# Optimization experiments

Hardware: AMD Instinct MI355X
Metric: run time of the kernel (lower is better)

## Reference

```python
import jax, jax.numpy as jnp
import numpy as np


def _conv_bn_relu(x, w, b, stride):
    # Conv2d(k=3, pad=1) with eval-mode BatchNorm folded into (w, b) at setup, then ReLU.
    y = jax.lax.conv_general_dilated(x, w, (stride, stride), ((1, 1), (1, 1)),
                                     dimension_numbers=('NCHW', 'OIHW', 'NCHW'))
    return jax.nn.relu(y + b[None, :, None, None])


def _affine_grid(theta, H, W):
    # torch.nn.functional.affine_grid, align_corners=False
    xs = (2.0 * jnp.arange(W, dtype=theta.dtype) + 1.0) / W - 1.0  # [W]
    ys = (2.0 * jnp.arange(H, dtype=theta.dtype) + 1.0) / H - 1.0  # [H]
    gx = theta[:, 0, 0, None, None] * xs[None, None, :] + theta[:, 0, 1, None, None] * ys[None, :, None] + theta[:, 0, 2, None, None]
    gy = theta[:, 1, 0, None, None] * xs[None, None, :] + theta[:, 1, 1, None, None] * ys[None, :, None] + theta[:, 1, 2, None, None]
    return jnp.stack([gx, gy], axis=-1)  # [B,H,W,2]


def _grid_sample_bilinear_zeros(im, grid):
    # torch.nn.functional.grid_sample, mode='bilinear', padding_mode='zeros', align_corners=False
    B, C, H, W = im.shape
    ix = ((grid[..., 0] + 1.0) * W - 1.0) * 0.5  # [B,H,W] pixel x coords
    iy = ((grid[..., 1] + 1.0) * H - 1.0) * 0.5
    x0 = jnp.floor(ix); y0 = jnp.floor(iy)
    x1 = x0 + 1.0;      y1 = y0 + 1.0
    wx1 = ix - x0; wx0 = 1.0 - wx1
    wy1 = iy - y0; wy0 = 1.0 - wy1
    imt = jnp.transpose(im, (0, 2, 3, 1))  # BHWC for channel-last gather
    bidx = jnp.arange(B)[:, None, None]

    def gather(xf, yf):
        valid = ((xf >= 0) & (xf <= W - 1) & (yf >= 0) & (yf <= H - 1)).astype(im.dtype)
        xi = jnp.clip(xf.astype(jnp.int32), 0, W - 1)
        yi = jnp.clip(yf.astype(jnp.int32), 0, H - 1)
        return imt[bidx, yi, xi] * valid[..., None]  # [B,H,W,C]

    out = (gather(x0, y0) * (wx0 * wy0)[..., None]
           + gather(x1, y0) * (wx1 * wy0)[..., None]
           + gather(x0, y1) * (wx0 * wy1)[..., None]
           + gather(x1, y1) * (wx1 * wy1)[..., None])
    return jnp.transpose(out, (0, 3, 1, 2))  # back to NCHW


def _forward(im_tensor, w1, b1, w2, b2, w3, b3, w4, b4, w5, b5, w6, b6,
             fw1, fb1, fw2, fb2, fw3, fb3):
    B, _, H, W = im_tensor.shape
    x1 = _conv_bn_relu(im_tensor, w1, b1, 1)
    x2 = _conv_bn_relu(jnp.concatenate([x1, im_tensor], 1), w2, b2, 2)
    x3 = _conv_bn_relu(x2, w3, b3, 1)
    x4 = _conv_bn_relu(jnp.concatenate([x3, x2], 1), w4, b4, 2)
    x5 = _conv_bn_relu(x4, w5, b5, 1)
    xs = _conv_bn_relu(jnp.concatenate([x5, x4], 1), w6, b6, 2)
    xs = xs.reshape(B, -1)  # [B, 24*(H/8)*(W/8)]
    h = jax.nn.relu(xs @ fw1.T + fb1)
    h = jax.nn.relu(h @ fw2.T + fb2)
    sz = h @ fw3.T + fb3  # [B, 4]
    # mode == 'normal': vectorized theta construction (original loops over batch)
    theta = jnp.zeros((B, 2, 3), dtype=im_tensor.dtype)
    theta = theta.at[:, 0, 0].set(jax.nn.sigmoid(sz[:, 0]))
    theta = theta.at[:, 0, 2].set(jnp.tanh(sz[:, 2]))
    theta = theta.at[:, 1, 1].set(jax.nn.sigmoid(sz[:, 1]))
    theta = theta.at[:, 1, 2].set(jnp.tanh(sz[:, 3]))
    grid = _affine_grid(theta, H, W)
    im_cropped = _grid_sample_bilinear_zeros(im_tensor, grid)
    return im_cropped, theta


def setup_inputs() -> dict:
    key = jax.random.key(0)
    B, H, W = 32, 256, 256
    keys = iter(jax.random.split(key, 64))
    nk = lambda: next(keys)
    im = jax.random.normal(nk(), (B, 1, H, W), jnp.float32)

    def conv_params(cin, cout):
        w = jax.random.normal(nk(), (cout, cin, 3, 3), jnp.float32) * (1.0 / np.sqrt(cin * 9))
        b = jax.random.normal(nk(), (cout,), jnp.float32) * 0.01
        # eval-mode BatchNorm params, folded into conv weight/bias (exact same math)
        gamma = 1.0 + 0.1 * jax.random.normal(nk(), (cout,), jnp.float32)
        beta = 0.1 * jax.random.normal(nk(), (cout,), jnp.float32)
        mean = 0.1 * jax.random.normal(nk(), (cout,), jnp.float32)
        var = jnp.abs(1.0 + 0.1 * jax.random.normal(nk(), (cout,), jnp.float32))
        scale = gamma / jnp.sqrt(var + 1e-5)
        return w * scale[:, None, None, None], b * scale + (beta - mean * scale)

    w1, b1 = conv_params(1, 8)
    w2, b2 = conv_params(9, 8)
    w3, b3 = conv_params(8, 16)
    w4, b4 = conv_params(24, 16)
    w5, b5 = conv_params(16, 24)
    w6, b6 = conv_params(40, 24)
    feat = 24 * (H // 8) * (W // 8)
    fw1 = jax.random.normal(nk(), (1024, feat), jnp.float32) * (1.0 / np.sqrt(feat))
    fb1 = jnp.zeros((1024,), jnp.float32)
    fw2 = jax.random.normal(nk(), (32, 1024), jnp.float32) * (1.0 / np.sqrt(1024))
    fb2 = jnp.zeros((32,), jnp.float32)
    fw3 = jax.random.normal(nk(), (4, 32), jnp.float32) * 0.01  # small perturbation of zero-init
    fb3 = jnp.array([1.0, 1.0, 0.0, 0.0], jnp.float32)
    return dict(im_tensor=im, w1=w1, b1=b1, w2=w2, b2=b2, w3=w3, b3=b3,
                w4=w4, b4=b4, w5=w5, b5=b5, w6=w6, b6=b6,
                fw1=fw1, fb1=fb1, fw2=fw2, fb2=fb2, fw3=fw3, fb3=fb3)


def reference(im_tensor, w1, b1, w2, b2, w3, b3, w4, b4, w5, b5, w6, b6,
              fw1, fb1, fw2, fb2, fw3, fb3):
    return _forward(im_tensor, w1, b1, w2, b2, w3, b3, w4, b4, w5, b5, w6, b6,
                    fw1, fb1, fw2, fb2, fw3, fb3)
```

## Files before the change

kernel.cpp:

```cpp
#include <hip/hip_runtime.h>
#include <hip/hip_bf16.h>

template <int CIN1, int CIN2, int COUT, int CG, int STRIDE, int CCH, int MINW>
__global__ __launch_bounds__(256, MINW) void conv2p_k(
    const float* __restrict__ in1, const float* __restrict__ in2,
    const float* __restrict__ w,
    const float* __restrict__ bias,
    float* __restrict__ out,
    int Hin, int Win)
{
    constexpr int CIN = CIN1 + CIN2;
    constexpr int NG  = COUT / CG;
    constexpr int NCH = CIN / CCH;
    constexpr int P   = 16 * STRIDE + 2;
    constexpr int NF4 = (STRIDE == 1) ? 10 : 17;
    constexpr int WL  = NF4 * 4;
    constexpr int E4  = CCH * P * NF4;
    constexpr int NLD = (E4 + 255) / 256;
    __shared__ __align__(16) float Xs[2][CCH][P][WL];

    const int Ho = Hin / STRIDE, Wo = Win / STRIDE;
    const int tpr = Wo / 32, tpc = Ho / 16;
    int bid = blockIdx.x;
    const int tx = bid % tpr; bid /= tpr;
    const int ty = bid % tpc; bid /= tpc;
    const int g  = bid % NG;  bid /= NG;
    const int b  = bid;
    const int cbase = g * CG;

    const int tid = threadIdx.x;
    const int lx = tid & 15, ly = tid >> 4;

    const int y0 = ty * 16 * STRIDE - 1;
    const int xA = tx * 32 * STRIDE - 4;
    const int HW = Hin * Win;

    float2 acc[CG];
#pragma unroll
    for (int co = 0; co < CG; ++co) {
        float bv = bias[cbase + co];
        acc[co].x = bv; acc[co].y = bv;
    }

    int cA[NLD], lOff[NLD], em[NLD];
    bool eok[NLD], rowk[NLD], f4[NLD];
    const float* b1p[NLD];
    const float* b2p[NLD];
#pragma unroll
    for (int l = 0; l < NLD; ++l) {
        int e = tid + l * 256;
        eok[l] = (e < E4);
        int ee = eok[l] ? e : 0;
        int c  = ee / (P * NF4), r = ee % (P * NF4);
        int py = r / NF4,        jx = r % NF4;
        cA[l]   = c;
        lOff[l] = ee;
        int gy = y0 + py, c0 = xA + jx * 4;
        rowk[l] = eok[l] && ((unsigned)gy < (unsigned)Hin);
        f4[l]   = (c0 >= 0) && (c0 + 4 <= Win);
        em[l] = 0;
#pragma unroll
        for (int e2 = 0; e2 < 4; ++e2)
            if ((unsigned)(c0 + e2) < (unsigned)Win) em[l] |= 1 << e2;
        b1p[l] = (const float*)((const char*)in1 +
                 ((ptrdiff_t)(b * CIN1 + c) * HW + (ptrdiff_t)gy * Win + c0)
                 * (ptrdiff_t)sizeof(float));
        b2p[l] = (CIN2 > 0)
            ? (const float*)((const char*)in2 +
                 ((ptrdiff_t)(b * CIN2 + c - CIN1) * HW + (ptrdiff_t)gy * Win + c0)
                 * (ptrdiff_t)sizeof(float))
            : b1p[l];
    }

    float4 stg[NLD];

    auto issue = [&](int cc) {
        const size_t adv = (size_t)cc * HW;
#pragma unroll
        for (int l = 0; l < NLD; ++l) {
            float4 v = {0.0f, 0.0f, 0.0f, 0.0f};
            if (rowk[l]) {
                int ci = cc + cA[l];
                const float* p = (CIN2 == 0 || ci < CIN1) ? (b1p[l] + adv)
                                                          : (b2p[l] + adv);
                if (f4[l]) {
                    v = *(const float4*)p;
                } else {
                    float* vp = reinterpret_cast<float*>(&v);
#pragma unroll
                    for (int e2 = 0; e2 < 4; ++e2)
                        if (em[l] & (1 << e2)) vp[e2] = p[e2];
                }
            }
            stg[l] = v;
        }
    };
    auto commit = [&](int bf) {
        float4* dst = (float4*)&Xs[0][0][0][0] + (size_t)bf * (CCH * P * NF4);
#pragma unroll
        for (int l = 0; l < NLD; ++l)
            if (eok[l]) dst[lOff[l]] = stg[l];
    };

    issue(0);
    commit(0);
    __syncthreads();

    const int cb = (2 * lx) * STRIDE + 3;

    int buf = 0;
    for (int ch = 0; ch < NCH; ++ch) {
        if (ch + 1 < NCH) issue((ch + 1) * CCH);
#pragma unroll
        for (int c = 0; c < CCH; ++c) {
#pragma unroll
            for (int ky = 0; ky < 3; ++ky) {
                const float* xr = &Xs[buf][c][ly * STRIDE + ky][0];
                float2 r0, r1, r2;
                r0.x = xr[cb + 0]; r0.y = xr[cb + 0 + STRIDE];
                r1.x = xr[cb + 1]; r1.y = xr[cb + 1 + STRIDE];
                r2.x = xr[cb + 2]; r2.y = xr[cb + 2 + STRIDE];
#pragma unroll
                for (int co = 0; co < CG; ++co) {
                    const float* wp = w +
                        ((size_t)(cbase + co) * CIN + ch * CCH + c) * 9 + ky * 3;
                    float w0 = wp[0], w1 = wp[1], w2 = wp[2];
                    float2 a = acc[co];
                    a.x = fmaf(r0.x, w0, a.x); a.y = fmaf(r0.y, w0, a.y);
                    a.x = fmaf(r1.x, w1, a.x); a.y = fmaf(r1.y, w1, a.y);
                    a.x = fmaf(r2.x, w2, a.x); a.y = fmaf(r2.y, w2, a.y);
                    acc[co] = a;
                }
            }
        }
        if (ch + 1 < NCH) {
            commit(buf ^ 1);
            __syncthreads();
            buf ^= 1;
        }
    }

    const int oy = ty * 16 + ly;
    const int ox = tx * 32 + 2 * lx;
#pragma unroll
    for (int co = 0; co < CG; ++co) {
        float2 v;
        v.x = fmaxf(acc[co].x, 0.0f);
        v.y = fmaxf(acc[co].y, 0.0f);
        *(float2*)&out[((size_t)(b * COUT + cbase + co) * Ho + oy) * Wo + ox] = v;
    }
}

#define FC1_K 24576
#define FC1_N 1024
#define FC1_M 32
#define FC1_KS 32
#define FC1_KC 768
#define FC1_KP 64
#define FC1_NT 64

__global__ __launch_bounds__(256) void fc1_stage_k(
    const float* __restrict__ xs,
    const float* __restrict__ fw1,
    float* __restrict__ part)
{
    __shared__ __align__(16) float As[FC1_KP][36];
    __shared__ __align__(16) float Bs[FC1_KP][66];

    const int tid = threadIdx.x;
    const int n0 = blockIdx.x * FC1_NT;
    const int ks = blockIdx.y;
    const int k0 = ks * FC1_KC;
    const int lane = tid & 63;
    const int grp = tid >> 6;

    const int m4 = (tid & 7) * 4;
    const int n2 = (tid >> 3) * 2;

    float acc[4][2];
#pragma unroll
    for (int i = 0; i < 4; ++i)
#pragma unroll
        for (int j = 0; j < 2; ++j) acc[i][j] = 0.0f;

    for (int p = 0; p < FC1_KC / FC1_KP; ++p) {
        const int kc = k0 + p * FC1_KP;
#pragma unroll
        for (int r = 0; r < 8; ++r) {
            int m = grp * 8 + r;
            As[lane][m] = xs[(size_t)m * FC1_K + kc + lane];
        }
#pragma unroll
        for (int r = 0; r < 16; ++r) {
            int nl = grp * 16 + r;
            Bs[lane][nl] = fw1[(size_t)(n0 + nl) * FC1_K + kc + lane];
        }
        __syncthreads();
#pragma unroll 8
        for (int k = 0; k < FC1_KP; ++k) {
            float4 a = *(const float4*)&As[k][m4];
            float2 bv = *(const float2*)&Bs[k][n2];
            acc[0][0] += a.x * bv.x; acc[0][1] += a.x * bv.y;
            acc[1][0] += a.y * bv.x; acc[1][1] += a.y * bv.y;
            acc[2][0] += a.z * bv.x; acc[2][1] += a.z * bv.y;
            acc[3][0] += a.w * bv.x; acc[3][1] += a.w * bv.y;
        }
        __syncthreads();
    }
#pragma unroll
    for (int i = 0; i < 4; ++i)
#pragma unroll
        for (int j = 0; j < 2; ++j)
            part[((size_t)ks * FC1_M + (m4 + i)) * FC1_N + n0 + n2 + j] = acc[i][j];
}

__global__ __launch_bounds__(256) void fc1_reduce_k(
    const float* __restrict__ part, const float* __restrict__ fb1,
    float* __restrict__ h1)
{
    int idx = blockIdx.x * 256 + threadIdx.x;
    int n = idx & (FC1_N - 1);
    int m = idx >> 10;
    float s = fb1[n];
#pragma unroll
    for (int ks = 0; ks < FC1_KS; ++ks)
        s += part[((size_t)ks * FC1_M + m) * FC1_N + n];
    h1[idx] = fmaxf(s, 0.0f);
}

__global__ __launch_bounds__(256) void fc2_k(
    const float* __restrict__ h1, const float* __restrict__ fw2,
    const float* __restrict__ fb2, float* __restrict__ h2)
{
    __shared__ float hs[1024];
    const int m = blockIdx.x;
    const int tid = threadIdx.x;
    for (int i = tid; i < 1024; i += 256) hs[i] = h1[m * 1024 + i];
    __syncthreads();
    const int wave = tid >> 6, lane = tid & 63;
#pragma unroll 1
    for (int nn = 0; nn < 8; ++nn) {
        int n = wave * 8 + nn;
        float p = 0.0f;
        for (int k = lane; k < 1024; k += 64)
            p += fw2[n * 1024 + k] * hs[k];
#pragma unroll
        for (int off = 32; off; off >>= 1) p += __shfl_xor(p, off);
        if (lane == 0) h2[m * 32 + n] = fmaxf(p + fb2[n], 0.0f);
    }
}

__global__ void fc3_theta_k(
    const float* __restrict__ h2, const float* __restrict__ fw3,
    const float* __restrict__ fb3, float* __restrict__ theta_out)
{
    int t = threadIdx.x;
    if (t >= 128) return;
    int m = t >> 2, j = t & 3;
    float s = fb3[j];
#pragma unroll
    for (int k = 0; k < 32; ++k) s += h2[m * 32 + k] * fw3[j * 32 + k];
    float* th = theta_out + m * 6;
    if (j == 0)      { th[0] = 1.0f / (1.0f + expf(-s)); th[1] = 0.0f; }
    else if (j == 1) { th[4] = 1.0f / (1.0f + expf(-s)); th[3] = 0.0f; }
    else if (j == 2) { th[2] = tanhf(s); }
    else             { th[5] = tanhf(s); }
}

__global__ __launch_bounds__(256) void sampler_k(
    const float* __restrict__ im, const float* __restrict__ theta,
    float* __restrict__ out)
{
    int idx = blockIdx.x * 256 + threadIdx.x;
    int x = idx & 255;
    int y = (idx >> 8) & 255;
    int b = idx >> 16;
    const float* th = theta + b * 6;
    float xsn = (2.0f * x + 1.0f) * (1.0f / 256.0f) - 1.0f;
    float ysn = (2.0f * y + 1.0f) * (1.0f / 256.0f) - 1.0f;
    float gx = th[0] * xsn + th[1] * ysn + th[2];
    float gy = th[3] * xsn + th[4] * ysn + th[5];
    float ix = ((gx + 1.0f) * 256.0f - 1.0f) * 0.5f;
    float iy = ((gy + 1.0f) * 256.0f - 1.0f) * 0.5f;
    float x0 = floorf(ix), y0 = floorf(iy);
    float wx1 = ix - x0, wy1 = iy - y0;
    float wx0 = 1.0f - wx1, wy0 = 1.0f - wy1;
    const float* src = im + (size_t)b * 65536;

    auto g = [&](float xf, float yf) -> float {
        if (xf < 0.0f || xf > 255.0f || yf < 0.0f || yf > 255.0f) return 0.0f;
        int xi = (int)xf, yi = (int)yf;
        return src[yi * 256 + xi];
    };
    float v00 = g(x0, y0);
    float v10 = g(x0 + 1.0f, y0);
    float v01 = g(x0, y0 + 1.0f);
    float v11 = g(x0 + 1.0f, y0 + 1.0f);
    out[idx] = v00 * wx0 * wy0 + v10 * wx1 * wy0 + v01 * wx0 * wy1 + v11 * wx1 * wy1;
}

extern "C" void kernel_launch(void* const* d_in, const int* in_sizes, int n_in,
                              void* d_out, int out_size, void* d_ws, size_t ws_size,
                              hipStream_t stream)
{
    const float* im  = (const float*)d_in[0];
    const float* w1  = (const float*)d_in[1];  const float* b1 = (const float*)d_in[2];
    const float* w2  = (const float*)d_in[3];  const float* b2 = (const float*)d_in[4];
    const float* w3  = (const float*)d_in[5];  const float* b3 = (const float*)d_in[6];
    const float* w4  = (const float*)d_in[7];  const float* b4 = (const float*)d_in[8];
    const float* w5  = (const float*)d_in[9];  const float* b5 = (const float*)d_in[10];
    const float* w6  = (const float*)d_in[11]; const float* b6 = (const float*)d_in[12];
    const float* fw1 = (const float*)d_in[13]; const float* fb1 = (const float*)d_in[14];
    const float* fw2 = (const float*)d_in[15]; const float* fb2 = (const float*)d_in[16];
    const float* fw3 = (const float*)d_in[17]; const float* fb3 = (const float*)d_in[18];

    float* out = (float*)d_out;
    float* ws  = (float*)d_ws;

    float* x2   = ws + 0;
    float* x1c  = ws + 4194304;
    float* x3   = ws + 4194304;
    float* x4   = ws + 12582912;
    float* x5   = ws + 4194304;
    float* x6   = ws + 14680064;
    float* part = ws + 0;
    float* h1   = ws + 1048576;
    float* h2   = ws + 1081344;

    float* theta = out + 32 * 65536;

    for (int c = 0; c < 2; ++c) {
        const float* imc = im + (size_t)c * 16 * 65536;
        conv2p_k<1, 0, 8, 8, 1, 1, 6><<<16 * 16 * 8, 256, 0, stream>>>(
            imc, nullptr, w1, b1, x1c, 256, 256);
        conv2p_k<8, 1, 8, 8, 2, 1, 6><<<16 * 8 * 4, 256, 0, stream>>>(
            x1c, imc, w2, b2, x2 + (size_t)c * 2097152, 256, 256);
    }
    conv2p_k<8, 0, 16, 8, 1, 2, 6><<<32 * 8 * 4 * 2, 256, 0, stream>>>(
        x2, nullptr, w3, b3, x3, 128, 128);
    conv2p_k<16, 8, 16, 4, 2, 1, 6><<<32 * 4 * 2 * 4, 256, 0, stream>>>(
        x3, x2, w4, b4, x4, 128, 128);
    conv2p_k<16, 0, 24, 8, 1, 2, 6><<<32 * 4 * 2 * 3, 256, 0, stream>>>(
        x4, nullptr, w5, b5, x5, 64, 64);
    conv2p_k<24, 16, 24, 4, 2, 1, 6><<<32 * 2 * 1 * 6, 256, 0, stream>>>(
        x5, x4, w6, b6, x6, 64, 64);

    fc1_stage_k<<<dim3(16, FC1_KS), 256, 0, stream>>>(x6, fw1, part);
    fc1_reduce_k<<<128, 256, 0, stream>>>(part, fb1, h1);
    fc2_k<<<32, 256, 0, stream>>>(h1, fw2, fb2, h2);
    fc3_theta_k<<<1, 128, 0, stream>>>(h2, fw3, fb3, theta);

    sampler_k<<<8192, 256, 0, stream>>>(im, theta, out);
}
```

Before: 301.3 us.

## Add 2x2-output-per-thread conv kernel for stride-1 layers

```diff
diff --git a/kernel.cpp b/kernel.cpp
--- a/kernel.cpp
+++ b/kernel.cpp
@@ -1,5 +1,164 @@
 #include <hip/hip_runtime.h>
 #include <hip/hip_bf16.h>
+
+template <int CIN1, int CIN2, int COUT, int CG, int CCH, int MINW>
+__global__ __launch_bounds__(256, MINW) void convq_k(
+    const float* __restrict__ in1, const float* __restrict__ in2,
+    const float* __restrict__ w,
+    const float* __restrict__ bias,
+    float* __restrict__ out,
+    int Hin, int Win)
+{
+    constexpr int CIN = CIN1 + CIN2;
+    constexpr int NG  = COUT / CG;
+    constexpr int NCH = CIN / CCH;
+    constexpr int P   = 34;
+    constexpr int NF4 = 10;
+    constexpr int WL  = NF4 * 4;
+    constexpr int E4  = CCH * P * NF4;
+    constexpr int NLD = (E4 + 255) / 256;
+    __shared__ __align__(16) float Xs[2][CCH][P][WL];
+
+    const int Ho = Hin, Wo = Win;
+    const int tpr = Wo / 32, tpc = Ho / 32;
+    int bid = blockIdx.x;
+    const int tx = bid % tpr; bid /= tpr;
+    const int ty = bid % tpc; bid /= tpc;
+    const int g  = bid % NG;  bid /= NG;
+    const int b  = bid;
+    const int cbase = g * CG;
+
+    const int tid = threadIdx.x;
+    const int lx = tid & 15, ly = tid >> 4;
+
+    const int y0 = ty * 32 - 1;
+    const int xA = tx * 32 - 4;
+    const int HW = Hin * Win;
+
+    float acc[CG][4];
+#pragma unroll
+    for (int co = 0; co < CG; ++co) {
+        float bv = bias[cbase + co];
+#pragma unroll
+        for (int p = 0; p < 4; ++p) acc[co][p] = bv;
+    }
+
+    int cA[NLD], lOff[NLD], em[NLD];
+    bool eok[NLD], rowk[NLD], f4[NLD];
+    const float* b1p[NLD];
+    const float* b2p[NLD];
+#pragma unroll
+    for (int l = 0; l < NLD; ++l) {
+        int e = tid + l * 256;
+        eok[l] = (e < E4);
+        int ee = eok[l] ? e : 0;
+        int c  = ee / (P * NF4), r = ee % (P * NF4);
+        int py = r / NF4,        jx = r % NF4;
+        cA[l]   = c;
+        lOff[l] = ee;
+        int gy = y0 + py, c0 = xA + jx * 4;
+        rowk[l] = eok[l] && ((unsigned)gy < (unsigned)Hin);
+        f4[l]   = (c0 >= 0) && (c0 + 4 <= Win);
+        em[l] = 0;
+#pragma unroll
+        for (int e2 = 0; e2 < 4; ++e2)
+            if ((unsigned)(c0 + e2) < (unsigned)Win) em[l] |= 1 << e2;
+        b1p[l] = (const float*)((const char*)in1 +
+                 ((ptrdiff_t)(b * CIN1 + c) * HW + (ptrdiff_t)gy * Win + c0)
+                 * (ptrdiff_t)sizeof(float));
+        b2p[l] = (CIN2 > 0)
+            ? (const float*)((const char*)in2 +
+                 ((ptrdiff_t)(b * CIN2 + c - CIN1) * HW + (ptrdiff_t)gy * Win + c0)
+                 * (ptrdiff_t)sizeof(float))
+            : b1p[l];
+    }
+
+    float4 stg[NLD];
+
+    auto issue = [&](int cc) {
+        const size_t adv = (size_t)cc * HW;
+#pragma unroll
+        for (int l = 0; l < NLD; ++l) {
+            float4 v = {0.0f, 0.0f, 0.0f, 0.0f};
+            if (rowk[l]) {
+                int ci = cc + cA[l];
+                const float* p = (CIN2 == 0 || ci < CIN1) ? (b1p[l] + adv)
+                                                          : (b2p[l] + adv);
+                if (f4[l]) {
+                    v = *(const float4*)p;
+                } else {
+                    float* vp = reinterpret_cast<float*>(&v);
+#pragma unroll
+                    for (int e2 = 0; e2 < 4; ++e2)
+                        if (em[l] & (1 << e2)) vp[e2] = p[e2];
+                }
+            }
+            stg[l] = v;
+        }
+    };
+    auto commit = [&](int bf) {
+        float4* dst = (float4*)&Xs[0][0][0][0] + (size_t)bf * (CCH * P * NF4);
+#pragma unroll
+        for (int l = 0; l < NLD; ++l)
+            if (eok[l]) dst[lOff[l]] = stg[l];
+    };
+
+    issue(0);
+    commit(0);
+    __syncthreads();
+
+    const int cb = 2 * lx + 3;
+
+    int buf = 0;
+    for (int ch = 0; ch < NCH; ++ch) {
+        if (ch + 1 < NCH) issue((ch + 1) * CCH);
+#pragma unroll
+        for (int c = 0; c < CCH; ++c) {
+#pragma unroll
+            for (int ky = 0; ky < 3; ++ky) {
+                const float* x0 = &Xs[buf][c][2 * ly + ky][cb];
+                const float* x1 = &Xs[buf][c][2 * ly + ky + 1][cb];
+                float a0 = x0[0], a1 = x0[1], a2 = x0[2], a3 = x0[3];
+                float b0 = x1[0], b1v = x1[1], b2v = x1[2], b3 = x1[3];
+#pragma unroll
+                for (int co = 0; co < CG; ++co) {
+                    const float* wp = w +
+                        ((size_t)(cbase + co) * CIN + ch * CCH + c) * 9 + ky * 3;
+                    float w0 = wp[0], w1 = wp[1], w2 = wp[2];
+                    acc[co][0] = fmaf(a0, w0, acc[co][0]);
+                    acc[co][0] = fmaf(a1, w1, acc[co][0]);
+                    acc[co][0] = fmaf(a2, w2, acc[co][0]);
+                    acc[co][1] = fmaf(a1, w0, acc[co][1]);
+                    acc[co][1] = fmaf(a2, w1, acc[co][1]);
+                    acc[co][1] = fmaf(a3, w2, acc[co][1]);
+                    acc[co][2] = fmaf(b0, w0, acc[co][2]);
+                    acc[co][2] = fmaf(b1v, w1, acc[co][2]);
+                    acc[co][2] = fmaf(b2v, w2, acc[co][2]);
+                    acc[co][3] = fmaf(b1v, w0, acc[co][3]);
+                    acc[co][3] = fmaf(b2v, w1, acc[co][3]);
+                    acc[co][3] = fmaf(b3, w2, acc[co][3]);
+                }
+            }
+        }
+        if (ch + 1 < NCH) {
+            commit(buf ^ 1);
+            __syncthreads();
+            buf ^= 1;
+        }
+    }
+
+    const int oy = ty * 32 + 2 * ly;
+    const int ox = tx * 32 + 2 * lx;
+#pragma unroll
+    for (int co = 0; co < CG; ++co)
+#pragma unroll
+        for (int dy = 0; dy < 2; ++dy) {
+            float2 v;
+            v.x = fmaxf(acc[co][dy * 2 + 0], 0.0f);
+            v.y = fmaxf(acc[co][dy * 2 + 1], 0.0f);
+            *(float2*)&out[((size_t)(b * COUT + cbase + co) * Ho + oy + dy) * Wo + ox] = v;
+        }
+}
 
 template <int CIN1, int CIN2, int COUT, int CG, int STRIDE, int CCH, int MINW>
 __global__ __launch_bounds__(256, MINW) void conv2p_k(
@@ -331,16 +490,16 @@
 
     for (int c = 0; c < 2; ++c) {
         const float* imc = im + (size_t)c * 16 * 65536;
-        conv2p_k<1, 0, 8, 8, 1, 1, 6><<<16 * 16 * 8, 256, 0, stream>>>(
+        convq_k<1, 0, 8, 8, 1, 4><<<16 * 1 * 8 * 8, 256, 0, stream>>>(
             imc, nullptr, w1, b1, x1c, 256, 256);
         conv2p_k<8, 1, 8, 8, 2, 1, 6><<<16 * 8 * 4, 256, 0, stream>>>(
             x1c, imc, w2, b2, x2 + (size_t)c * 2097152, 256, 256);
     }
-    conv2p_k<8, 0, 16, 8, 1, 2, 6><<<32 * 8 * 4 * 2, 256, 0, stream>>>(
+    convq_k<8, 0, 16, 8, 2, 4><<<32 * 2 * 4 * 4, 256, 0, stream>>>(
         x2, nullptr, w3, b3, x3, 128, 128);
     conv2p_k<16, 8, 16, 4, 2, 1, 6><<<32 * 4 * 2 * 4, 256, 0, stream>>>(
         x3, x2, w4, b4, x4, 128, 128);
-    conv2p_k<16, 0, 24, 8, 1, 2, 6><<<32 * 4 * 2 * 3, 256, 0, stream>>>(
+    convq_k<16, 0, 24, 6, 2, 4><<<32 * 4 * 2 * 2, 256, 0, stream>>>(
         x4, nullptr, w5, b5, x5, 64, 64);
     conv2p_k<24, 16, 24, 4, 2, 1, 6><<<32 * 2 * 1 * 6, 256, 0, stream>>>(
         x5, x4, w6, b6, x6, 64, 64);
```

New measurement: 281.8 us. 6.5% less time.
